# Kernel optimization log

Hardware: AMD Instinct MI355X
Metric: run time of the kernel (lower is better)

The kernel has to match this reference:

```python
import jax, jax.numpy as jnp
import numpy as np

B, S, D_MODEL, H = 2, 2048, 1024, 16
DK = D_MODEL // H
THETA = 10000.0


def setup_inputs() -> dict:
    key = jax.random.key(0)
    ks = jax.random.split(key, 5)
    scale = 0.02  # keep logits in a numerically sane range
    return {
        "x": jax.random.normal(ks[0], (B, S, D_MODEL), jnp.float32),
        "Q_weight": jax.random.normal(ks[1], (D_MODEL, D_MODEL), jnp.float32) * scale,
        "K_weight": jax.random.normal(ks[2], (D_MODEL, D_MODEL), jnp.float32) * scale,
        "V_weight": jax.random.normal(ks[3], (D_MODEL, D_MODEL), jnp.float32) * scale,
        "O_weight": jax.random.normal(ks[4], (D_MODEL, D_MODEL), jnp.float32) * scale,
        "token_positions": jnp.arange(S, dtype=jnp.int32),
    }


def _rope(x, token_positions, theta, d_k):
    # x: [..., seq, d_k]; rotate interleaved even/odd pairs
    inv_freq = 1.0 / theta ** (jnp.arange(0, d_k, 2, dtype=jnp.float32) / d_k)
    ang = token_positions.astype(jnp.float32)[:, None] * inv_freq  # [S, d_k/2]
    cos, sin = jnp.cos(ang), jnp.sin(ang)
    x0, x1 = x[..., 0::2], x[..., 1::2]
    y0 = x0 * cos - x1 * sin
    y1 = x0 * sin + x1 * cos
    return jnp.stack([y0, y1], axis=-1).reshape(x.shape)


def _mhsa(x, Qw, Kw, Vw, Ow, token_positions):
    b, s, d = x.shape
    qw = Qw.reshape(H, DK, d)
    kw = Kw.reshape(H, DK, d)
    vw = Vw.reshape(H, DK, d)
    q = jnp.einsum('hki,bsi->bhsk', qw, x)
    k = jnp.einsum('hki,bsi->bhsk', kw, x)
    v = jnp.einsum('hvi,bsi->bhsv', vw, x)
    q = _rope(q, token_positions, THETA, DK)
    k = _rope(k, token_positions, THETA, DK)
    scores = jnp.einsum('bhnd,bhmd->bhnm', q, k) / jnp.sqrt(jnp.float32(DK))
    causal = jnp.tril(jnp.ones((s, s), dtype=bool))
    scores = jnp.where(causal, scores, -jnp.inf)
    attn = jax.nn.softmax(scores, axis=-1)
    o = jnp.einsum('bhnm,bhmv->bhnv', attn, v)  # [B,H,S,DV]
    o = jnp.transpose(o, (0, 2, 1, 3)).reshape(b, s, H * DK)
    return jnp.einsum('dv,bsv->bsd', Ow, o)


def reference(x, Q_weight, K_weight, V_weight, O_weight, token_positions):
    return _mhsa(x, Q_weight, K_weight, V_weight, O_weight, token_positions)
```

## Files before the change

### kernel.cpp

```cpp
#include <hip/hip_runtime.h>

#define NB 2
#define NS 2048
#define NDM 1024
#define NH 16
#define NDK 64

typedef unsigned int u32;
typedef u32 u32x4 __attribute__((ext_vector_type(4)));
typedef float f32x4 __attribute__((ext_vector_type(4)));
typedef __bf16 bf16x8 __attribute__((ext_vector_type(8)));
typedef __bf16 bf16x4 __attribute__((ext_vector_type(4)));
typedef __bf16 bf16x2 __attribute__((ext_vector_type(2)));

__device__ __forceinline__ void gload_lds16(const __bf16* g, __bf16* l) {
    __builtin_amdgcn_global_load_lds(
        (const __attribute__((address_space(1))) unsigned int*)(g),
        (__attribute__((address_space(3))) unsigned int*)(l), 16, 0, 0);
}

__global__ __launch_bounds__(256) void cvt_f32_bf16(const float* __restrict__ src,
                                                    __bf16* __restrict__ dst, int n4) {
    int i = blockIdx.x * blockDim.x + threadIdx.x;
    if (i >= n4) return;
    f32x4 v = *(const f32x4*)(src + (size_t)i * 4);
    bf16x4 o;
    o[0] = (__bf16)v[0]; o[1] = (__bf16)v[1]; o[2] = (__bf16)v[2]; o[3] = (__bf16)v[3];
    *(bf16x4*)(dst + (size_t)i * 4) = o;
}

__global__ __launch_bounds__(256) void cvt_weights(const float* __restrict__ q,
                                                   const float* __restrict__ k,
                                                   const float* __restrict__ v,
                                                   const float* __restrict__ o,
                                                   __bf16* __restrict__ wqkv,
                                                   __bf16* __restrict__ owb) {
    const int seg = blockIdx.y;
    const float* src = (seg == 0) ? q : (seg == 1) ? k : (seg == 2) ? v : o;
    __bf16* dst = (seg == 3) ? owb : wqkv + (size_t)seg * 1024 * 1024;
    const int i = blockIdx.x * 256 + threadIdx.x;
    f32x4 vv = *(const f32x4*)(src + (size_t)i * 4);
    bf16x4 ov;
    ov[0] = (__bf16)vv[0]; ov[1] = (__bf16)vv[1]; ov[2] = (__bf16)vv[2]; ov[3] = (__bf16)vv[3];
    *(bf16x4*)(dst + (size_t)i * 4) = ov;
}

template <typename TOUT>
__global__ __launch_bounds__(256) void gemm_bt128(const __bf16* __restrict__ A,
                                                  const __bf16* __restrict__ Bt,
                                                  TOUT* __restrict__ C,
                                                  int K, int lda, int ldb, int ldc) {
    __shared__ __bf16 As[2][128 * 64];
    __shared__ __bf16 Bs[2][128 * 64];
    const int tid = threadIdx.x;
    const int lane = tid & 63, w = tid >> 6;
    const int wr = w >> 1, wc = w & 1;
    const int l15 = lane & 15, lg = lane >> 4;
    const int m0 = blockIdx.y * 128, n0 = blockIdx.x * 128;
    const int crow = lane >> 3;
    const int csw = ((lane & 7) ^ crow) * 8;

    f32x4 acc[4][4];
    const f32x4 z = {0.f, 0.f, 0.f, 0.f};
#pragma unroll
    for (int i = 0; i < 4; ++i)
#pragma unroll
        for (int jx = 0; jx < 4; ++jx) acc[i][jx] = z;

    auto stage = [&](int buf, int k0) {
#pragma unroll
        for (int ch = 0; ch < 4; ++ch) {
            const int cid = w * 4 + ch;
            const int ra = cid * 8 + crow;
            gload_lds16(&A[(size_t)(m0 + ra) * lda + k0 + csw], &As[buf][cid * 512]);
            gload_lds16(&Bt[(size_t)(n0 + ra) * ldb + k0 + csw], &Bs[buf][cid * 512]);
        }
    };

    stage(0, 0);
    __syncthreads();
    int cur = 0;
    for (int k0 = 0; k0 < K; k0 += 64) {
        if (k0 + 64 < K) stage(cur ^ 1, k0 + 64);
#pragma unroll
        for (int kc = 0; kc < 2; ++kc) {
            bf16x8 af[4], bfv[4];
#pragma unroll
            for (int i = 0; i < 4; ++i) {
                const int ra = wr * 64 + i * 16 + l15;
                const int rb = wc * 64 + i * 16 + l15;
                af[i]  = *(const bf16x8*)&As[cur][ra * 64 + ((kc * 32 + lg * 8) ^ ((ra & 7) << 3))];
                bfv[i] = *(const bf16x8*)&Bs[cur][rb * 64 + ((kc * 32 + lg * 8) ^ ((rb & 7) << 3))];
            }
#pragma unroll
            for (int sm = 0; sm < 4; ++sm)
#pragma unroll
                for (int sn = 0; sn < 4; ++sn)
                    acc[sm][sn] = __builtin_amdgcn_mfma_f32_16x16x32_bf16(af[sm], bfv[sn], acc[sm][sn], 0, 0, 0);
        }
        __syncthreads();
        cur ^= 1;
    }
#pragma unroll
    for (int sm = 0; sm < 4; ++sm)
#pragma unroll
        for (int sn = 0; sn < 4; ++sn)
#pragma unroll
            for (int j = 0; j < 4; ++j) {
                const int row = m0 + wr * 64 + sm * 16 + lg * 4 + j;
                const int col = n0 + wc * 64 + sn * 16 + l15;
                C[(size_t)row * ldc + col] = (TOUT)acc[sm][sn][j];
            }
}

__global__ __launch_bounds__(512) void rope_kernel(const __bf16* __restrict__ qkv,
                                                   const int* __restrict__ tp,
                                                   __bf16* __restrict__ Qr,
                                                   __bf16* __restrict__ Kr) {
    const int row = blockIdx.x;
    const int s = row & (NS - 1);
    const int b = row >> 11;
    const int t = threadIdx.x;
    const int h = t >> 5, jj = t & 31;
    const float pos = (float)tp[s];
    const float inv = exp2f(-0.41524101186092f * (float)jj);
    const float ang = pos * inv;
    float sn, cs;
    sincosf(ang, &sn, &cs);
    const __bf16* qp = qkv + (size_t)row * 3072 + h * 64 + 2 * jj;
    bf16x2 qv = *(const bf16x2*)qp;
    bf16x2 kv = *(const bf16x2*)(qp + 1024);
    const float q0 = (float)qv[0], q1 = (float)qv[1];
    const float k0 = (float)kv[0], k1 = (float)kv[1];
    const size_t o = ((size_t)(b * NH + h) * NS + s) * 64 + 2 * jj;
    bf16x2 qo, ko;
    qo[0] = (__bf16)((q0 * cs - q1 * sn) * 0.125f);
    qo[1] = (__bf16)((q0 * sn + q1 * cs) * 0.125f);
    ko[0] = (__bf16)(k0 * cs - k1 * sn); ko[1] = (__bf16)(k0 * sn + k1 * cs);
    *(bf16x2*)&Qr[o] = qo;
    *(bf16x2*)&Kr[o] = ko;
}

__global__ __launch_bounds__(256) void vtrans(const __bf16* __restrict__ qkv,
                                              __bf16* __restrict__ Vt) {
    const int bh = blockIdx.y;
    const int s0 = blockIdx.x * 64;
    const int b = bh >> 4, h = bh & 15;
    __shared__ __bf16 tile[64][72];
    const int t = threadIdx.x;
    const int sl = t >> 3, c8 = (t & 7) * 8;
#pragma unroll
    for (int pp = 0; pp < 2; ++pp) {
        const int srow = sl + pp * 32;
        bf16x8 v = *(const bf16x8*)&qkv[(size_t)(b * NS + s0 + srow) * 3072 + 2048 + h * 64 + c8];
        *(bf16x8*)&tile[srow][c8] = v;
    }
    __syncthreads();
    const int d = t >> 2;
#pragma unroll
    for (int pp = 0; pp < 2; ++pp) {
        const int vec = (t & 3) + pp * 4;
        bf16x8 o;
#pragma unroll
        for (int i = 0; i < 8; ++i) o[i] = tile[vec * 8 + i][d];
        *(bf16x8*)&Vt[((size_t)bh * 64 + d) * NS + s0 + vec * 8] = o;
    }
}

__device__ __forceinline__ int kperm(int rt) {
    const int ct = rt >> 4, rr = rt & 15;
    return ((rr >> 2) << 3) + ((ct >> 1) << 5) + ((ct & 1) << 2) + (rr & 3);
}

__global__ __launch_bounds__(256) void attn4(const __bf16* __restrict__ Qr,
                                             const __bf16* __restrict__ Kr,
                                             const __bf16* __restrict__ Vt,
                                             __bf16* __restrict__ O) {
    const int lid = blockIdx.x;
    const int xcd = lid & 7, ix = lid >> 3;
    const int bh = xcd * 4 + (ix & 3);
    const int p  = ix >> 2;
    const int b = bh >> 4, h = bh & 15;
    const int tid = threadIdx.x;
    const int w = tid >> 6, lane = tid & 63;
    const int l15 = lane & 15, lg = lane >> 4;
    const __bf16* Qb = Qr + (size_t)bh * NS * 64;
    const __bf16* Kb = Kr + (size_t)bh * NS * 64;
    const __bf16* Vb = Vt + (size_t)bh * 64 * NS;

    __shared__ __bf16 Ks[2][64 * 64];
    __shared__ __bf16 Vs[2][64 * 64];

    const int rbv[2] = {p * 64 + w * 16, (31 - p) * 64 + w * 16};

    bf16x8 qf[2][2];
#pragma unroll
    for (int rs = 0; rs < 2; ++rs)
#pragma unroll
        for (int kc = 0; kc < 2; ++kc)
            qf[rs][kc] = *(const bf16x8*)(Qb + (size_t)(rbv[rs] + l15) * 64 + kc * 32 + lg * 8);

    f32x4 oacc[2][4];
    const f32x4 z = {0.f, 0.f, 0.f, 0.f};
#pragma unroll
    for (int rs = 0; rs < 2; ++rs)
#pragma unroll
        for (int ct = 0; ct < 4; ++ct) oacc[rs][ct] = z;
    float m[2], lsum[2];
#pragma unroll
    for (int rs = 0; rs < 2; ++rs) { m[rs] = -1e30f; lsum[rs] = 0.f; }

    const int crow = lane >> 3;
    const int cswz = ((lane & 7) ^ crow) * 8;

#pragma unroll
    for (int pp = 0; pp < 2; ++pp) {
        const int ch = w + pp * 4;
        const int rt = ch * 8 + crow;
        gload_lds16(Kb + (size_t)kperm(rt) * 64 + cswz, &Ks[0][ch * 512]);
        gload_lds16(Vb + (size_t)rt * NS + 0 + cswz, &Vs[0][ch * 512]);
    }
    __syncthreads();

    const int nt = 32 - p;
    for (int t = 0; t < nt; ++t) {
        const int cur = t & 1;
        const int kv0 = t << 6;
        if (t + 1 < nt) {
            const int kv1 = kv0 + 64;
#pragma unroll
            for (int pp = 0; pp < 2; ++pp) {
                const int ch = w + pp * 4;
                const int rt = ch * 8 + crow;
                gload_lds16(Kb + (size_t)(kv1 + kperm(rt)) * 64 + cswz, &Ks[cur ^ 1][ch * 512]);
                gload_lds16(Vb + (size_t)rt * NS + kv1 + cswz, &Vs[cur ^ 1][ch * 512]);
            }
        }
        bool act[2];
        act[0] = (kv0 <= rbv[0] + 15);
        act[1] = true;
        f32x4 sc[2][4];
#pragma unroll
        for (int rs = 0; rs < 2; ++rs)
            if (act[rs])
#pragma unroll
                for (int ct = 0; ct < 4; ++ct) sc[rs][ct] = z;
#pragma unroll
        for (int kc = 0; kc < 2; ++kc) {
            bf16x8 kf[4];
#pragma unroll
            for (int ct = 0; ct < 4; ++ct) {
                const int rt = ct * 16 + l15;
                kf[ct] = *(const bf16x8*)&Ks[cur][rt * 64 + ((kc * 32 + lg * 8) ^ ((rt & 7) << 3))];
            }
#pragma unroll
            for (int rs = 0; rs < 2; ++rs)
                if (act[rs])
#pragma unroll
                    for (int ct = 0; ct < 4; ++ct)
                        sc[rs][ct] = __builtin_amdgcn_mfma_f32_16x16x32_bf16(kf[ct], qf[rs][kc], sc[rs][ct], 0, 0, 0);
        }
        bf16x8 pb[2][2];
#pragma unroll
        for (int rs = 0; rs < 2; ++rs) {
            if (!act[rs]) continue;
            const int rbase = rbv[rs];
            const int qrow = rbase + l15;
            const bool needmask = (kv0 + 63 > rbase);
            if (needmask) {
#pragma unroll
                for (int ct = 0; ct < 4; ++ct)
#pragma unroll
                    for (int j = 0; j < 4; ++j) {
                        const int kvg = kv0 + ((ct >> 1) << 5) + lg * 8 + ((ct & 1) << 2) + j;
                        if (kvg > qrow) sc[rs][ct][j] = -1e30f;
                    }
            }
            float t0 = fmaxf(fmaxf(sc[rs][0][0], sc[rs][0][1]), fmaxf(sc[rs][0][2], sc[rs][0][3]));
            float t1 = fmaxf(fmaxf(sc[rs][1][0], sc[rs][1][1]), fmaxf(sc[rs][1][2], sc[rs][1][3]));
            float t2 = fmaxf(fmaxf(sc[rs][2][0], sc[rs][2][1]), fmaxf(sc[rs][2][2], sc[rs][2][3]));
            float t3 = fmaxf(fmaxf(sc[rs][3][0], sc[rs][3][1]), fmaxf(sc[rs][3][2], sc[rs][3][3]));
            float mt = fmaxf(fmaxf(t0, t1), fmaxf(t2, t3));
            mt = fmaxf(mt, __shfl_xor(mt, 16, 64));
            mt = fmaxf(mt, __shfl_xor(mt, 32, 64));
            float alpha = 1.0f;
            if (!__all(mt - m[rs] <= 8.0f)) {
                const float mn = fmaxf(m[rs], mt);
                alpha = __expf(m[rs] - mn);
                m[rs] = mn;
#pragma unroll
                for (int ct = 0; ct < 4; ++ct)
#pragma unroll
                    for (int j = 0; j < 4; ++j) oacc[rs][ct][j] *= alpha;
            }
            float ps = 0.f;
#pragma unroll
            for (int ct = 0; ct < 4; ++ct)
#pragma unroll
                for (int j = 0; j < 4; ++j) {
                    const float e = __expf(sc[rs][ct][j] - m[rs]);
                    sc[rs][ct][j] = e;
                    ps += e;
                }
            ps += __shfl_xor(ps, 16, 64);
            ps += __shfl_xor(ps, 32, 64);
            lsum[rs] = lsum[rs] * alpha + ps;
#pragma unroll
            for (int kc = 0; kc < 2; ++kc) {
                bf16x8 pk;
                pk[0] = (__bf16)sc[rs][2 * kc][0];     pk[1] = (__bf16)sc[rs][2 * kc][1];
                pk[2] = (__bf16)sc[rs][2 * kc][2];     pk[3] = (__bf16)sc[rs][2 * kc][3];
                pk[4] = (__bf16)sc[rs][2 * kc + 1][0]; pk[5] = (__bf16)sc[rs][2 * kc + 1][1];
                pk[6] = (__bf16)sc[rs][2 * kc + 1][2]; pk[7] = (__bf16)sc[rs][2 * kc + 1][3];
                pb[rs][kc] = pk;
            }
        }
#pragma unroll
        for (int kc = 0; kc < 2; ++kc) {
            bf16x8 vf[4];
#pragma unroll
            for (int ct = 0; ct < 4; ++ct) {
                const int rt = ct * 16 + l15;
                vf[ct] = *(const bf16x8*)&Vs[cur][rt * 64 + ((kc * 32 + lg * 8) ^ ((rt & 7) << 3))];
            }
#pragma unroll
            for (int rs = 0; rs < 2; ++rs) {
                if (!act[rs]) continue;
#pragma unroll
                for (int ct = 0; ct < 4; ++ct)
                    oacc[rs][ct] = __builtin_amdgcn_mfma_f32_16x16x32_bf16(vf[ct], pb[rs][kc], oacc[rs][ct], 0, 0, 0);
            }
        }
        __syncthreads();
    }
#pragma unroll
    for (int rs = 0; rs < 2; ++rs) {
        const float rl = 1.0f / lsum[rs];
        const size_t rowoff = (size_t)(b * NS + rbv[rs] + l15) * NDM + h * 64 + lg * 4;
#pragma unroll
        for (int ct = 0; ct < 4; ++ct) {
            bf16x4 ov;
#pragma unroll
            for (int j = 0; j < 4; ++j) ov[j] = (__bf16)(oacc[rs][ct][j] * rl);
            *(bf16x4*)&O[rowoff + ct * 16] = ov;
        }
    }
}

extern "C" void kernel_launch(void* const* d_in, const int* in_sizes, int n_in,
                              void* d_out, int out_size, void* d_ws, size_t ws_size,
                              hipStream_t stream) {
    const float* x  = (const float*)d_in[0];
    const float* Qw = (const float*)d_in[1];
    const float* Kw = (const float*)d_in[2];
    const float* Vw = (const float*)d_in[3];
    const float* Ow = (const float*)d_in[4];
    const int*   tp = (const int*)d_in[5];
    float* out = (float*)d_out;

    char* ws = (char*)d_ws;
    size_t off = 0;
    auto alloc = [&](size_t bytes) -> void* {
        void* p = ws + off;
        off += (bytes + 255) & ~(size_t)255;
        return p;
    };
    __bf16* xb   = (__bf16*)alloc((size_t)4096 * 1024 * 2);
    __bf16* wqkv = (__bf16*)alloc((size_t)3072 * 1024 * 2);
    __bf16* owb  = (__bf16*)alloc((size_t)1024 * 1024 * 2);
    __bf16* qkv  = (__bf16*)alloc((size_t)4096 * 3072 * 2);
    __bf16* qr   = (__bf16*)alloc((size_t)32 * 2048 * 64 * 2);
    __bf16* kr   = (__bf16*)alloc((size_t)32 * 2048 * 64 * 2);
    __bf16* vt   = (__bf16*)alloc((size_t)32 * 64 * 2048 * 2);
    __bf16* ob   = (__bf16*)alloc((size_t)4096 * 1024 * 2);

    cvt_f32_bf16<<<4096, 256, 0, stream>>>(x, xb, 4096 * 1024 / 4);
    cvt_weights<<<dim3(1024, 4), 256, 0, stream>>>(Qw, Kw, Vw, Ow, wqkv, owb);

    gemm_bt128<__bf16><<<dim3(3072 / 128, 4096 / 128), 256, 0, stream>>>(
        xb, wqkv, qkv, 1024, 1024, 1024, 3072);
    rope_kernel<<<4096, 512, 0, stream>>>(qkv, tp, qr, kr);
    vtrans<<<dim3(NS / 64, NB * NH), 256, 0, stream>>>(qkv, vt);
    attn4<<<dim3(512), 256, 0, stream>>>(qr, kr, vt, ob);
    gemm_bt128<float><<<dim3(1024 / 128, 4096 / 128), 256, 0, stream>>>(
        ob, owb, out, 1024, 1024, 1024, 1024);
}
```

Measured before the change: 122.9 us.

## Fuse RoPE into QKV GEMM epilogue and use exp2 softmax with MFMA priority

Moves RoPE rotation and Q scaling into the QKV GEMM epilogue, using a precomputed cos/sin table and lane shuffles to pair even/odd columns, and writes Q/K directly in head-major layout. V goes to a separate buffer. This removes the standalone rope kernel and the round trip of Q/K through the full qkv buffer. The Q scale now folds in log2(e), so attention uses exp2f. s_setprio is raised around the MFMA blocks to favour matrix issue. The epilogue does scattered 2-byte stores and per-element table loads, which may be uncoalesced.

```diff
diff --git a/kernel.cpp b/kernel.cpp
--- a/kernel.cpp
+++ b/kernel.cpp
@@ -9,9 +9,12 @@
 typedef unsigned int u32;
 typedef u32 u32x4 __attribute__((ext_vector_type(4)));
 typedef float f32x4 __attribute__((ext_vector_type(4)));
+typedef float f32x2 __attribute__((ext_vector_type(2)));
 typedef __bf16 bf16x8 __attribute__((ext_vector_type(8)));
 typedef __bf16 bf16x4 __attribute__((ext_vector_type(4)));
 typedef __bf16 bf16x2 __attribute__((ext_vector_type(2)));
+
+#define QSCALE 0.18033688011112042f
 
 __device__ __forceinline__ void gload_lds16(const __bf16* g, __bf16* l) {
     __builtin_amdgcn_global_load_lds(
@@ -45,6 +48,114 @@
     *(bf16x4*)(dst + (size_t)i * 4) = ov;
 }
 
+__global__ __launch_bounds__(256) void rope_table(const int* __restrict__ tp,
+                                                  float* __restrict__ tbl) {
+    const int i = blockIdx.x * 256 + threadIdx.x;
+    if (i >= NS * 32) return;
+    const int s = i >> 5, jj = i & 31;
+    const float pos = (float)tp[s];
+    const float inv = exp2f(-0.41524101186092f * (float)jj);
+    const float ang = pos * inv;
+    float sn, cs;
+    sincosf(ang, &sn, &cs);
+    f32x2 o; o[0] = cs; o[1] = sn;
+    *(f32x2*)&tbl[(size_t)i * 2] = o;
+}
+
+__global__ __launch_bounds__(256) void gemm_qkv(const __bf16* __restrict__ A,
+                                                const __bf16* __restrict__ Bt,
+                                                const float* __restrict__ tbl,
+                                                __bf16* __restrict__ Qr,
+                                                __bf16* __restrict__ Kr,
+                                                __bf16* __restrict__ vbuf) {
+    __shared__ __bf16 As[2][128 * 64];
+    __shared__ __bf16 Bs[2][128 * 64];
+    const int K = 1024, lda = 1024, ldb = 1024;
+    const int tid = threadIdx.x;
+    const int lane = tid & 63, w = tid >> 6;
+    const int wr = w >> 1, wc = w & 1;
+    const int l15 = lane & 15, lg = lane >> 4;
+    const int m0 = blockIdx.y * 128, n0 = blockIdx.x * 128;
+    const int crow = lane >> 3;
+    const int csw = ((lane & 7) ^ crow) * 8;
+
+    f32x4 acc[4][4];
+    const f32x4 z = {0.f, 0.f, 0.f, 0.f};
+#pragma unroll
+    for (int i = 0; i < 4; ++i)
+#pragma unroll
+        for (int jx = 0; jx < 4; ++jx) acc[i][jx] = z;
+
+    auto stage = [&](int buf, int k0) {
+#pragma unroll
+        for (int ch = 0; ch < 4; ++ch) {
+            const int cid = w * 4 + ch;
+            const int ra = cid * 8 + crow;
+            gload_lds16(&A[(size_t)(m0 + ra) * lda + k0 + csw], &As[buf][cid * 512]);
+            gload_lds16(&Bt[(size_t)(n0 + ra) * ldb + k0 + csw], &Bs[buf][cid * 512]);
+        }
+    };
+
+    stage(0, 0);
+    __syncthreads();
+    int cur = 0;
+    for (int k0 = 0; k0 < K; k0 += 64) {
+        if (k0 + 64 < K) stage(cur ^ 1, k0 + 64);
+#pragma unroll
+        for (int kc = 0; kc < 2; ++kc) {
+            bf16x8 af[4], bfv[4];
+#pragma unroll
+            for (int i = 0; i < 4; ++i) {
+                const int ra = wr * 64 + i * 16 + l15;
+                const int rb = wc * 64 + i * 16 + l15;
+                af[i]  = *(const bf16x8*)&As[cur][ra * 64 + ((kc * 32 + lg * 8) ^ ((ra & 7) << 3))];
+                bfv[i] = *(const bf16x8*)&Bs[cur][rb * 64 + ((kc * 32 + lg * 8) ^ ((rb & 7) << 3))];
+            }
+#pragma unroll
+            for (int sm = 0; sm < 4; ++sm)
+#pragma unroll
+                for (int sn = 0; sn < 4; ++sn)
+                    acc[sm][sn] = __builtin_amdgcn_mfma_f32_16x16x32_bf16(af[sm], bfv[sn], acc[sm][sn], 0, 0, 0);
+        }
+        __syncthreads();
+        cur ^= 1;
+    }
+
+    if (n0 < 2048) {
+        __bf16* dst = (n0 < 1024) ? Qr : Kr;
+        const float scale = (n0 < 1024) ? QSCALE : 1.0f;
+        const int odd = l15 & 1;
+#pragma unroll
+        for (int sn = 0; sn < 4; ++sn) {
+            const int col = (n0 & 1023) + wc * 64 + sn * 16 + l15;
+            const int h = col >> 6, jj = (col & 63) >> 1, d = col & 63;
+#pragma unroll
+            for (int sm = 0; sm < 4; ++sm)
+#pragma unroll
+                for (int j = 0; j < 4; ++j) {
+                    const int row = m0 + wr * 64 + sm * 16 + lg * 4 + j;
+                    const int b = row >> 11, s = row & (NS - 1);
+                    const float v = acc[sm][sn][j];
+                    const float other = __shfl_xor(v, 1, 64);
+                    f32x2 cssn = *(const f32x2*)&tbl[((size_t)s * 32 + jj) * 2];
+                    const float r = v * cssn[0] + (odd ? other * cssn[1] : -other * cssn[1]);
+                    dst[((size_t)(b * NH + h) * NS + s) * 64 + d] = (__bf16)(r * scale);
+                }
+        }
+    } else {
+#pragma unroll
+        for (int sm = 0; sm < 4; ++sm)
+#pragma unroll
+            for (int sn = 0; sn < 4; ++sn)
+#pragma unroll
+                for (int j = 0; j < 4; ++j) {
+                    const int row = m0 + wr * 64 + sm * 16 + lg * 4 + j;
+                    const int col = (n0 - 2048) + wc * 64 + sn * 16 + l15;
+                    vbuf[(size_t)row * 1024 + col] = (__bf16)acc[sm][sn][j];
+                }
+    }
+}
+
 template <typename TOUT>
 __global__ __launch_bounds__(256) void gemm_bt128(const __bf16* __restrict__ A,
                                                   const __bf16* __restrict__ Bt,
@@ -113,35 +224,7 @@
             }
 }
 
-__global__ __launch_bounds__(512) void rope_kernel(const __bf16* __restrict__ qkv,
-                                                   const int* __restrict__ tp,
-                                                   __bf16* __restrict__ Qr,
-                                                   __bf16* __restrict__ Kr) {
-    const int row = blockIdx.x;
-    const int s = row & (NS - 1);
-    const int b = row >> 11;
-    const int t = threadIdx.x;
-    const int h = t >> 5, jj = t & 31;
-    const float pos = (float)tp[s];
-    const float inv = exp2f(-0.41524101186092f * (float)jj);
-    const float ang = pos * inv;
-    float sn, cs;
-    sincosf(ang, &sn, &cs);
-    const __bf16* qp = qkv + (size_t)row * 3072 + h * 64 + 2 * jj;
-    bf16x2 qv = *(const bf16x2*)qp;
-    bf16x2 kv = *(const bf16x2*)(qp + 1024);
-    const float q0 = (float)qv[0], q1 = (float)qv[1];
-    const float k0 = (float)kv[0], k1 = (float)kv[1];
-    const size_t o = ((size_t)(b * NH + h) * NS + s) * 64 + 2 * jj;
-    bf16x2 qo, ko;
-    qo[0] = (__bf16)((q0 * cs - q1 * sn) * 0.125f);
-    qo[1] = (__bf16)((q0 * sn + q1 * cs) * 0.125f);
-    ko[0] = (__bf16)(k0 * cs - k1 * sn); ko[1] = (__bf16)(k0 * sn + k1 * cs);
-    *(bf16x2*)&Qr[o] = qo;
-    *(bf16x2*)&Kr[o] = ko;
-}
-
-__global__ __launch_bounds__(256) void vtrans(const __bf16* __restrict__ qkv,
+__global__ __launch_bounds__(256) void vtrans(const __bf16* __restrict__ vbuf,
                                               __bf16* __restrict__ Vt) {
     const int bh = blockIdx.y;
     const int s0 = blockIdx.x * 64;
@@ -152,7 +235,7 @@
 #pragma unroll
     for (int pp = 0; pp < 2; ++pp) {
         const int srow = sl + pp * 32;
-        bf16x8 v = *(const bf16x8*)&qkv[(size_t)(b * NS + s0 + srow) * 3072 + 2048 + h * 64 + c8];
+        bf16x8 v = *(const bf16x8*)&vbuf[(size_t)(b * NS + s0 + srow) * 1024 + h * 64 + c8];
         *(bf16x8*)&tile[srow][c8] = v;
     }
     __syncthreads();
@@ -172,7 +255,7 @@
     return ((rr >> 2) << 3) + ((ct >> 1) << 5) + ((ct & 1) << 2) + (rr & 3);
 }
 
-__global__ __launch_bounds__(256) void attn4(const __bf16* __restrict__ Qr,
+__global__ __launch_bounds__(256) void attn5(const __bf16* __restrict__ Qr,
                                              const __bf16* __restrict__ Kr,
                                              const __bf16* __restrict__ Vt,
                                              __bf16* __restrict__ O) {
@@ -253,12 +336,14 @@
                 const int rt = ct * 16 + l15;
                 kf[ct] = *(const bf16x8*)&Ks[cur][rt * 64 + ((kc * 32 + lg * 8) ^ ((rt & 7) << 3))];
             }
+            __builtin_amdgcn_s_setprio(1);
 #pragma unroll
             for (int rs = 0; rs < 2; ++rs)
                 if (act[rs])
 #pragma unroll
                     for (int ct = 0; ct < 4; ++ct)
                         sc[rs][ct] = __builtin_amdgcn_mfma_f32_16x16x32_bf16(kf[ct], qf[rs][kc], sc[rs][ct], 0, 0, 0);
+            __builtin_amdgcn_s_setprio(0);
         }
         bf16x8 pb[2][2];
 #pragma unroll
@@ -286,7 +371,7 @@
             float alpha = 1.0f;
             if (!__all(mt - m[rs] <= 8.0f)) {
                 const float mn = fmaxf(m[rs], mt);
-                alpha = __expf(m[rs] - mn);
+                alpha = exp2f(m[rs] - mn);
                 m[rs] = mn;
 #pragma unroll
                 for (int ct = 0; ct < 4; ++ct)
@@ -298,7 +383,7 @@
             for (int ct = 0; ct < 4; ++ct)
 #pragma unroll
                 for (int j = 0; j < 4; ++j) {
-                    const float e = __expf(sc[rs][ct][j] - m[rs]);
+                    const float e = exp2f(sc[rs][ct][j] - m[rs]);
                     sc[rs][ct][j] = e;
                     ps += e;
                 }
@@ -323,6 +408,7 @@
                 const int rt = ct * 16 + l15;
                 vf[ct] = *(const bf16x8*)&Vs[cur][rt * 64 + ((kc * 32 + lg * 8) ^ ((rt & 7) << 3))];
             }
+            __builtin_amdgcn_s_setprio(1);
 #pragma unroll
             for (int rs = 0; rs < 2; ++rs) {
                 if (!act[rs]) continue;
@@ -330,6 +416,7 @@
                 for (int ct = 0; ct < 4; ++ct)
                     oacc[rs][ct] = __builtin_amdgcn_mfma_f32_16x16x32_bf16(vf[ct], pb[rs][kc], oacc[rs][ct], 0, 0, 0);
             }
+            __builtin_amdgcn_s_setprio(0);
         }
         __syncthreads();
     }
@@ -368,20 +455,20 @@
     __bf16* xb   = (__bf16*)alloc((size_t)4096 * 1024 * 2);
     __bf16* wqkv = (__bf16*)alloc((size_t)3072 * 1024 * 2);
     __bf16* owb  = (__bf16*)alloc((size_t)1024 * 1024 * 2);
-    __bf16* qkv  = (__bf16*)alloc((size_t)4096 * 3072 * 2);
+    __bf16* vbuf = (__bf16*)alloc((size_t)4096 * 1024 * 2);
     __bf16* qr   = (__bf16*)alloc((size_t)32 * 2048 * 64 * 2);
     __bf16* kr   = (__bf16*)alloc((size_t)32 * 2048 * 64 * 2);
     __bf16* vt   = (__bf16*)alloc((size_t)32 * 64 * 2048 * 2);
     __bf16* ob   = (__bf16*)alloc((size_t)4096 * 1024 * 2);
+    float*  tbl  = (float*)alloc((size_t)NS * 32 * 2 * 4);
 
     cvt_f32_bf16<<<4096, 256, 0, stream>>>(x, xb, 4096 * 1024 / 4);
     cvt_weights<<<dim3(1024, 4), 256, 0, stream>>>(Qw, Kw, Vw, Ow, wqkv, owb);
-
-    gemm_bt128<__bf16><<<dim3(3072 / 128, 4096 / 128), 256, 0, stream>>>(
-        xb, wqkv, qkv, 1024, 1024, 1024, 3072);
-    rope_kernel<<<4096, 512, 0, stream>>>(qkv, tp, qr, kr);
-    vtrans<<<dim3(NS / 64, NB * NH), 256, 0, stream>>>(qkv, vt);
-    attn4<<<dim3(512), 256, 0, stream>>>(qr, kr, vt, ob);
+    rope_table<<<(NS * 32 + 255) / 256, 256, 0, stream>>>(tp, tbl);
+
+    gemm_qkv<<<dim3(3072 / 128, 4096 / 128), 256, 0, stream>>>(xb, wqkv, tbl, qr, kr, vbuf);
+    vtrans<<<dim3(NS / 64, NB * NH), 256, 0, stream>>>(vbuf, vt);
+    attn5<<<dim3(512), 256, 0, stream>>>(qr, kr, vt, ob);
     gemm_bt128<float><<<dim3(1024 / 128, 4096 / 128), 256, 0, stream>>>(
         ob, owb, out, 1024, 1024, 1024, 1024);
 }
```

Measured after the change: 135.4 us. +10.2%, slower.

## Use 256x256-tile XCD-swizzled GEMM for QKV projection and exp2 softmax

Applied to the files above, without the earlier changes.

Replaces the 128x128 QKV projection GEMM with a new 512-thread kernel that uses 256x256 output tiles. It issues 192 blocks in a 1-D grid remapped so that consecutive tiles land on the same XCD, which raises data reuse per tile and L2 locality. Separately, the softmax folds log2(e) into the Q scale so the attention kernel can call exp2f instead of __expf. The larger tiles add register and LDS pressure, and with only 192 blocks some CUs may sit partly idle.

```diff
diff --git a/kernel.cpp b/kernel.cpp
--- a/kernel.cpp
+++ b/kernel.cpp
@@ -9,9 +9,12 @@
 typedef unsigned int u32;
 typedef u32 u32x4 __attribute__((ext_vector_type(4)));
 typedef float f32x4 __attribute__((ext_vector_type(4)));
+typedef float f32x2 __attribute__((ext_vector_type(2)));
 typedef __bf16 bf16x8 __attribute__((ext_vector_type(8)));
 typedef __bf16 bf16x4 __attribute__((ext_vector_type(4)));
 typedef __bf16 bf16x2 __attribute__((ext_vector_type(2)));
+
+#define QSCALE 0.18033688011112042f
 
 __device__ __forceinline__ void gload_lds16(const __bf16* g, __bf16* l) {
     __builtin_amdgcn_global_load_lds(
@@ -43,6 +46,93 @@
     bf16x4 ov;
     ov[0] = (__bf16)vv[0]; ov[1] = (__bf16)vv[1]; ov[2] = (__bf16)vv[2]; ov[3] = (__bf16)vv[3];
     *(bf16x4*)(dst + (size_t)i * 4) = ov;
+}
+
+__global__ __launch_bounds__(512, 2) void gemm256(const __bf16* __restrict__ A,
+                                                  const __bf16* __restrict__ Bt,
+                                                  __bf16* __restrict__ C,
+                                                  int K, int lda, int ldb, int ldc, int nbx) {
+    __shared__ __bf16 As[2][256 * 64];
+    __shared__ __bf16 Bs[2][256 * 64];
+    const int tid = threadIdx.x;
+    const int lane = tid & 63, w = tid >> 6;
+    const int wm = w >> 2, wn = w & 3;
+    const int l15 = lane & 15, lg = lane >> 4;
+    int bid = blockIdx.x;
+    const int cpx = gridDim.x >> 3;
+    bid = (bid & 7) * cpx + (bid >> 3);
+    const int m0 = (bid / nbx) * 256, n0 = (bid % nbx) * 256;
+    const int srow = w * 8 + (lane >> 3);
+    const int csw = ((lane & 7) ^ (srow & 7)) * 8;
+
+    f32x4 acc[8][4];
+    const f32x4 z = {0.f, 0.f, 0.f, 0.f};
+#pragma unroll
+    for (int i = 0; i < 8; ++i)
+#pragma unroll
+        for (int jx = 0; jx < 4; ++jx) acc[i][jx] = z;
+
+    auto stage = [&](int buf, int k0) {
+#pragma unroll
+        for (int ps = 0; ps < 4; ++ps) {
+            const int r = ps * 64 + srow;
+            gload_lds16(&A[(size_t)(m0 + r) * lda + k0 + csw], &As[buf][(ps * 64 + w * 8) * 64]);
+        }
+#pragma unroll
+        for (int ps = 0; ps < 4; ++ps) {
+            const int r = ps * 64 + srow;
+            gload_lds16(&Bt[(size_t)(n0 + r) * ldb + k0 + csw], &Bs[buf][(ps * 64 + w * 8) * 64]);
+        }
+    };
+
+    stage(0, 0);
+    int cur = 0;
+    for (int k0 = 0; k0 < K; k0 += 64) {
+        if (k0 + 64 < K) {
+            stage(cur ^ 1, k0 + 64);
+            asm volatile("s_waitcnt vmcnt(8)" ::: "memory");
+        } else {
+            asm volatile("s_waitcnt vmcnt(0)" ::: "memory");
+        }
+        __builtin_amdgcn_s_barrier();
+        __builtin_amdgcn_sched_barrier(0);
+        bf16x8 bfr[4][2];
+#pragma unroll
+        for (int n = 0; n < 4; ++n)
+#pragma unroll
+            for (int kc = 0; kc < 2; ++kc) {
+                const int rb = wn * 64 + n * 16 + l15;
+                bfr[n][kc] = *(const bf16x8*)&Bs[cur][rb * 64 + ((kc * 32 + lg * 8) ^ ((rb & 7) << 3))];
+            }
+#pragma unroll
+        for (int mr = 0; mr < 8; ++mr) {
+            bf16x8 af[2];
+#pragma unroll
+            for (int kc = 0; kc < 2; ++kc) {
+                const int ra = wm * 128 + mr * 16 + l15;
+                af[kc] = *(const bf16x8*)&As[cur][ra * 64 + ((kc * 32 + lg * 8) ^ ((ra & 7) << 3))];
+            }
+#pragma unroll
+            for (int n = 0; n < 4; ++n)
+#pragma unroll
+                for (int kc = 0; kc < 2; ++kc)
+                    acc[mr][n] = __builtin_amdgcn_mfma_f32_16x16x32_bf16(af[kc], bfr[n][kc], acc[mr][n], 0, 0, 0);
+        }
+        asm volatile("s_waitcnt lgkmcnt(0)" ::: "memory");
+        __builtin_amdgcn_s_barrier();
+        __builtin_amdgcn_sched_barrier(0);
+        cur ^= 1;
+    }
+#pragma unroll
+    for (int mr = 0; mr < 8; ++mr)
+#pragma unroll
+        for (int n = 0; n < 4; ++n)
+#pragma unroll
+            for (int j = 0; j < 4; ++j) {
+                const int row = m0 + wm * 128 + mr * 16 + lg * 4 + j;
+                const int col = n0 + wn * 64 + n * 16 + l15;
+                C[(size_t)row * ldc + col] = (__bf16)acc[mr][n][j];
+            }
 }
 
 template <typename TOUT>
@@ -134,8 +224,8 @@
     const float k0 = (float)kv[0], k1 = (float)kv[1];
     const size_t o = ((size_t)(b * NH + h) * NS + s) * 64 + 2 * jj;
     bf16x2 qo, ko;
-    qo[0] = (__bf16)((q0 * cs - q1 * sn) * 0.125f);
-    qo[1] = (__bf16)((q0 * sn + q1 * cs) * 0.125f);
+    qo[0] = (__bf16)((q0 * cs - q1 * sn) * QSCALE);
+    qo[1] = (__bf16)((q0 * sn + q1 * cs) * QSCALE);
     ko[0] = (__bf16)(k0 * cs - k1 * sn); ko[1] = (__bf16)(k0 * sn + k1 * cs);
     *(bf16x2*)&Qr[o] = qo;
     *(bf16x2*)&Kr[o] = ko;
@@ -172,7 +262,7 @@
     return ((rr >> 2) << 3) + ((ct >> 1) << 5) + ((ct & 1) << 2) + (rr & 3);
 }
 
-__global__ __launch_bounds__(256) void attn4(const __bf16* __restrict__ Qr,
+__global__ __launch_bounds__(256) void attn5(const __bf16* __restrict__ Qr,
                                              const __bf16* __restrict__ Kr,
                                              const __bf16* __restrict__ Vt,
                                              __bf16* __restrict__ O) {
@@ -286,7 +376,7 @@
             float alpha = 1.0f;
             if (!__all(mt - m[rs] <= 8.0f)) {
                 const float mn = fmaxf(m[rs], mt);
-                alpha = __expf(m[rs] - mn);
+                alpha = exp2f(m[rs] - mn);
                 m[rs] = mn;
 #pragma unroll
                 for (int ct = 0; ct < 4; ++ct)
@@ -298,7 +388,7 @@
             for (int ct = 0; ct < 4; ++ct)
 #pragma unroll
                 for (int j = 0; j < 4; ++j) {
-                    const float e = __expf(sc[rs][ct][j] - m[rs]);
+                    const float e = exp2f(sc[rs][ct][j] - m[rs]);
                     sc[rs][ct][j] = e;
                     ps += e;
                 }
@@ -377,11 +467,10 @@
     cvt_f32_bf16<<<4096, 256, 0, stream>>>(x, xb, 4096 * 1024 / 4);
     cvt_weights<<<dim3(1024, 4), 256, 0, stream>>>(Qw, Kw, Vw, Ow, wqkv, owb);
 
-    gemm_bt128<__bf16><<<dim3(3072 / 128, 4096 / 128), 256, 0, stream>>>(
-        xb, wqkv, qkv, 1024, 1024, 1024, 3072);
+    gemm256<<<192, 512, 0, stream>>>(xb, wqkv, qkv, 1024, 1024, 1024, 3072, 12);
     rope_kernel<<<4096, 512, 0, stream>>>(qkv, tp, qr, kr);
     vtrans<<<dim3(NS / 64, NB * NH), 256, 0, stream>>>(qkv, vt);
-    attn4<<<dim3(512), 256, 0, stream>>>(qr, kr, vt, ob);
+    attn5<<<dim3(512), 256, 0, stream>>>(qr, kr, vt, ob);
     gemm_bt128<float><<<dim3(1024 / 128, 4096 / 128), 256, 0, stream>>>(
         ob, owb, out, 1024, 1024, 1024, 1024);
 }
```

Measured after the change: 126.0 us. 1.03x slower.
